# Performance work log

Hardware: AMD Instinct MI355X
Metric: run time of the kernel (lower is better)

The kernel has to match this reference:

```python
import jax, jax.numpy as jnp
import numpy as np

E = 8        # num_experts
TOP_K = 2
DIM = 1024
DFF = DIM // 4
T = 32768    # batch*seq tokens


def setup_inputs() -> dict:
    key = jax.random.key(0)
    ks = jax.random.split(key, 5)
    x = jax.random.normal(ks[0], (T, DIM), dtype=jnp.float32)
    router_w = jax.random.normal(ks[1], (E, DIM), dtype=jnp.float32) * 0.02
    w1 = jax.random.normal(ks[2], (E, DIM, DFF), dtype=jnp.float32) * 0.02
    w2 = jax.random.normal(ks[3], (E, DFF, DIM), dtype=jnp.float32) * 0.02
    w3 = jax.random.normal(ks[4], (E, DIM, DFF), dtype=jnp.float32) * 0.02
    return {"x": x, "router_w": router_w, "w1": w1, "w2": w2, "w3": w3}


def reference(x, router_w, w1, w2, w3):
    # ---- Router ----
    logits = x @ router_w.T                          # [T, E]
    scores = jax.nn.softmax(logits.astype(jnp.float32), axis=1)
    # expert_bias is zero at init and noise_scale=0 -> topk on raw scores
    _, sel = jax.lax.top_k(scores, TOP_K)            # [T, K] expert indices
    top_scores = jnp.take_along_axis(scores, sel, axis=-1)
    top_scores = top_scores / jnp.sum(top_scores, axis=-1, keepdims=True)

    flat_experts = sel.reshape(-1)                   # [T*K]
    sorted_idx = jnp.argsort(flat_experts)           # stable sort, expert-centric order
    scatter_idx = sorted_idx // TOP_K                # original token id per row
    num_tokens_per_expert = jnp.bincount(flat_experts, length=E).astype(jnp.int32)

    x_gathered = x[scatter_idx]                      # [T*K, DIM]
    scores_sorted = top_scores.reshape(-1)[sorted_idx]  # [T*K]

    # ---- GroupedExpert: grouped GEMM SwiGLU in bf16 ----
    xb = x_gathered.astype(jnp.bfloat16)
    x1 = jax.lax.ragged_dot(xb, w1.astype(jnp.bfloat16), num_tokens_per_expert)
    x3 = jax.lax.ragged_dot(xb, w3.astype(jnp.bfloat16), num_tokens_per_expert)
    h = jax.nn.silu(x1) * x3                         # [T*K, DFF] bf16
    expert_out = jax.lax.ragged_dot(h, w2.astype(jnp.bfloat16), num_tokens_per_expert)
    expert_out = expert_out.astype(x.dtype)          # [T*K, DIM]

    # ---- Combine: weighted scatter-add back to token positions ----
    out = jnp.zeros_like(x).at[scatter_idx].add(expert_out * scores_sorted[:, None])
    return out
```

## Files before the change

kernel.cpp:

```cpp
#include <hip/hip_runtime.h>
#include <cstdint>
#include <cstddef>
#include <math.h>

#define T_TOK 32768
#define DIM   1024
#define DFF   256
#define NE    8
#define NB    16
#define ROWS  (T_TOK * 2)
#define MAXROWS 66560
#define MAXTILES (MAXROWS / 64)

typedef unsigned short u16;
typedef __attribute__((ext_vector_type(8))) short v8s;
typedef __attribute__((ext_vector_type(4))) float v4f;

__device__ __forceinline__ u16 f2bf(float f) {
  union { float f; unsigned u; } v; v.f = f;
  return (u16)((v.u + 0x7FFFu + ((v.u >> 16) & 1u)) >> 16);
}
__device__ __forceinline__ float bf2f(u16 b) {
  union { unsigned u; float f; } v; v.u = ((unsigned)b) << 16; return v.f;
}

__device__ __forceinline__ void gload16(const u16* g, u16* l) {
  __builtin_amdgcn_global_load_lds(
      (const __attribute__((address_space(1))) void*)g,
      (__attribute__((address_space(3))) void*)l, 16, 0, 0);
}

#define WS_W13  ((size_t)0)
#define WS_W2T  ((size_t)8388608)
#define WS_H    ((size_t)12582912)
#define WS_Y    ((size_t)46661632)
#define WS_RTOK ((size_t)182976512)
#define WS_POS  ((size_t)183242752)
#define WS_CNT  ((size_t)183504896)
#define WS_CUR  ((size_t)183504960)
#define WS_OFF  ((size_t)183505024)
#define WS_SEL  ((size_t)183505152)
#define WS_WTS  ((size_t)183767296)
#define WS_XB   WS_Y

__global__ __launch_bounds__(256) void k_pack13(const float* __restrict__ w1,
                                                const float* __restrict__ w3,
                                                u16* __restrict__ W13p) {
  __shared__ float s1[32][33];
  __shared__ float s3[32][33];
  int e = blockIdx.z, k0 = blockIdx.x * 32, j0w = blockIdx.y;
  int tx = threadIdx.x, ty = threadIdx.y;
  size_t wbase = (size_t)e * DIM * DFF;
#pragma unroll
  for (int r = 0; r < 4; ++r) {
    int kl = ty + 8 * r;
    size_t src = wbase + (size_t)(k0 + kl) * DFF + j0w * 32 + tx;
    s1[kl][tx] = w1[src];
    s3[kl][tx] = w3[src];
  }
  __syncthreads();
  size_t obase = (size_t)e * 512 * 1024;
#pragma unroll
  for (int r = 0; r < 4; ++r) {
    int jl = ty + 8 * r;
    int n1 = 64 * j0w + jl;
    W13p[obase + (size_t)n1 * 1024 + k0 + tx]        = f2bf(s1[tx][jl]);
    W13p[obase + (size_t)(n1 + 32) * 1024 + k0 + tx] = f2bf(s3[tx][jl]);
  }
}

__global__ __launch_bounds__(256) void k_pack2(const float* __restrict__ w2,
                                               u16* __restrict__ W2t) {
  __shared__ float s[32][33];
  int e = blockIdx.z, k0 = blockIdx.x * 32, n0 = blockIdx.y * 32;
  int tx = threadIdx.x, ty = threadIdx.y;
#pragma unroll
  for (int r = 0; r < 4; ++r) {
    int kl = ty + 8 * r;
    s[kl][tx] = w2[(size_t)e * DFF * DIM + (size_t)(k0 + kl) * DIM + n0 + tx];
  }
  __syncthreads();
#pragma unroll
  for (int r = 0; r < 4; ++r) {
    int nl = ty + 8 * r;
    W2t[(size_t)e * DIM * DFF + (size_t)(n0 + nl) * DFF + k0 + tx] = f2bf(s[tx][nl]);
  }
}

__global__ __launch_bounds__(256) void k_router(const float* __restrict__ x,
                                                const float* __restrict__ rw,
                                                int* __restrict__ sel,
                                                float* __restrict__ wts,
                                                int* __restrict__ cnt,
                                                u16* __restrict__ xb) {
  __shared__ __align__(16) float s_rw[NE][1028];
  __shared__ __align__(16) float s_x[32][132];
  __shared__ float s_lg[256];
  __shared__ int s_cnt[NB];
  int tid = threadIdx.x;
  if (tid < NB) s_cnt[tid] = 0;
  {
    const float4* rw4 = (const float4*)rw;
#pragma unroll
    for (int r = 0; r < 8; ++r)
      *(float4*)(&s_rw[r][tid * 4]) = rw4[r * 256 + tid];
  }
  int tl = tid >> 3, e = tid & 7;
  float acc = 0.0f;
  const float4* x4 = (const float4*)x;
  for (int c = 0; c < 8; ++c) {
    __syncthreads();
#pragma unroll
    for (int j = 0; j < 4; ++j) {
      int slot = j * 256 + tid;
      int t = slot >> 5, kk = (slot & 31) * 4;
      *(float4*)(&s_x[t][kk]) = x4[((size_t)blockIdx.x * 32 + t) * 256 + c * 32 + (slot & 31)];
    }
    __syncthreads();
    const float* xp = &s_x[tl][0];
    const float* wp = &s_rw[e][c * 128];
#pragma unroll 16
    for (int k = 0; k < 128; ++k) acc = fmaf(xp[k], wp[k], acc);
    {
      int t2 = tid >> 3, k2 = (tid & 7) * 16;
      const float* sp = &s_x[t2][k2];
      u16 tb[16];
#pragma unroll
      for (int k = 0; k < 16; ++k) tb[k] = f2bf(sp[k]);
      u16* xo = xb + ((size_t)(blockIdx.x * 32 + t2)) * 1024 + c * 128 + k2;
      *(uint4*)(xo)     = *(const uint4*)(&tb[0]);
      *(uint4*)(xo + 8) = *(const uint4*)(&tb[8]);
    }
  }
  s_lg[tid] = acc;
  __syncthreads();
  if ((tid & 7) == 0) {
    int t = blockIdx.x * 32 + tl;
    const float* lg = s_lg + tid;
    int b0 = 0; float v0 = lg[0];
#pragma unroll
    for (int ee = 1; ee < NE; ++ee) if (lg[ee] > v0) { v0 = lg[ee]; b0 = ee; }
    int b1 = -1; float v1 = -1e30f;
#pragma unroll
    for (int ee = 0; ee < NE; ++ee) if (ee != b0 && lg[ee] > v1) { v1 = lg[ee]; b1 = ee; }
    float w0 = 1.0f / (1.0f + expf(v1 - v0));
    sel[2 * t] = b0; sel[2 * t + 1] = b1;
    wts[2 * t] = w0; wts[2 * t + 1] = 1.0f - w0;
    atomicAdd(&s_cnt[2 * b0], 1);
    atomicAdd(&s_cnt[2 * b1 + 1], 1);
  }
  __syncthreads();
  if (tid < NB && s_cnt[tid]) atomicAdd(&cnt[tid], s_cnt[tid]);
}

__global__ void k_scan(const int* __restrict__ cnt, int* __restrict__ offs) {
  if (threadIdx.x == 0 && blockIdx.x == 0) {
    int o = 0;
#pragma unroll
    for (int b = 0; b < NB; ++b) { offs[b] = o; o += (cnt[b] + 63) & ~63; }
    offs[NB] = o;
  }
}

__global__ __launch_bounds__(256) void k_scatter(const int* __restrict__ sel,
                                                 const int* __restrict__ offs,
                                                 int* __restrict__ cursor,
                                                 int* __restrict__ rtok,
                                                 int* __restrict__ pos) {
  __shared__ int s_cnt[NB], s_base[NB];
  int tid = threadIdx.x;
  if (tid < NB) s_cnt[tid] = 0;
  __syncthreads();
  int g = blockIdx.x * 256 + tid;
  int b = sel[g] * 2 + (g & 1);
  int lpos = atomicAdd(&s_cnt[b], 1);
  __syncthreads();
  if (tid < NB) s_base[tid] = s_cnt[tid] ? atomicAdd(&cursor[tid], s_cnt[tid]) : 0;
  __syncthreads();
  int row = offs[b] + s_base[b] + lpos;
  rtok[row] = g >> 1;
  pos[g] = row;
}

__global__ __launch_bounds__(512, 4) void k_gemm1(const u16* __restrict__ xb,
                                                  const u16* __restrict__ W13p,
                                                  const int* __restrict__ rtok,
                                                  const int* __restrict__ offs,
                                                  u16* __restrict__ h) {
  __shared__ __align__(16) u16 A_s[2][64][32];
  __shared__ __align__(16) u16 B_s[2][512][32];
  int bx = (int)((blockIdx.x & 7) * (MAXTILES / 8) + (blockIdx.x >> 3));
  int row0 = bx * 64;
  if (row0 >= offs[NB]) return;
  int b2 = 0;
  while (row0 >= offs[b2 + 1]) ++b2;
  int e = b2 >> 1;
  int tid = threadIdx.x;
  int wv = tid >> 6, lane = tid & 63;
  int lr = lane & 15, q = lane >> 4;
  int qa = q ^ ((lr >> 1) & 3);
  int srow = lane >> 2;
  int schk = (lane & 3) ^ ((lane >> 3) & 3);
  const u16* srcB = W13p + (size_t)e * 512 * 1024
                  + (size_t)(64 * wv + srow) * 1024 + schk * 8;
  int arow = (wv >= 4) ? (16 * (wv - 4) + srow) : srow;
  int tk = rtok[row0 + arow]; if (tk < 0) tk = 0;
  const u16* srcA = xb + (size_t)tk * 1024 + schk * 8;
  v4f acc[4][4] = {};

#define G1_STAGE(buf, k0) do {                                              \
    u16* ldsB_ = &B_s[buf][64 * wv][0];                                     \
    _Pragma("unroll")                                                       \
    for (int i_ = 0; i_ < 4; ++i_)                                          \
      gload16(srcB + (size_t)i_ * 16 * 1024 + (k0), ldsB_ + i_ * 512);      \
    if (wv >= 4) gload16(srcA + (k0), &A_s[buf][(wv & 3) * 16][0]);         \
  } while (0)

#define G1_COMP(buf) do {                                                   \
    v8s a_[4], b_[4];                                                       \
    _Pragma("unroll")                                                       \
    for (int mt_ = 0; mt_ < 4; ++mt_)                                       \
      a_[mt_] = *(const v8s*)(&A_s[buf][16 * mt_ + lr][qa * 8]);            \
    _Pragma("unroll")                                                       \
    for (int nt_ = 0; nt_ < 4; ++nt_)                                       \
      b_[nt_] = *(const v8s*)(&B_s[buf][64 * wv + 16 * nt_ + lr][qa * 8]);  \
    _Pragma("unroll")                                                       \
    for (int mt_ = 0; mt_ < 4; ++mt_)                                       \
      _Pragma("unroll")                                                     \
      for (int nt_ = 0; nt_ < 4; ++nt_)                                     \
        acc[mt_][nt_] = __builtin_amdgcn_mfma_f32_16x16x32_bf16(            \
            a_[mt_], b_[nt_], acc[mt_][nt_], 0, 0, 0);                      \
  } while (0)

  G1_STAGE(0, 0);
  asm volatile("s_waitcnt vmcnt(0)" ::: "memory");
  __builtin_amdgcn_s_barrier();
  __builtin_amdgcn_sched_barrier(0);
#pragma unroll 2
  for (int t = 0; t < 31; ++t) {
    int cur = t & 1;
    G1_STAGE(cur ^ 1, (t + 1) * 32);
    G1_COMP(cur);
    asm volatile("s_waitcnt vmcnt(0)" ::: "memory");
    __builtin_amdgcn_s_barrier();
    __builtin_amdgcn_sched_barrier(0);
  }
  G1_COMP(1);

#pragma unroll
  for (int mt = 0; mt < 4; ++mt)
#pragma unroll
    for (int nt = 0; nt < 2; ++nt)
#pragma unroll
      for (int r = 0; r < 4; ++r) {
        float x1 = bf2f(f2bf(acc[mt][nt][r]));
        float x3 = bf2f(f2bf(acc[mt][nt + 2][r]));
        float hv = x1 * x3 / (1.0f + __expf(-x1));
        int row = row0 + 16 * mt + q * 4 + r;
        int col = 32 * wv + 16 * nt + lr;
        h[(size_t)row * DFF + col] = f2bf(hv);
      }
#undef G1_STAGE
#undef G1_COMP
}

__global__ __launch_bounds__(512, 4) void k_gemm2(const u16* __restrict__ h,
                                                  const u16* __restrict__ W2t,
                                                  const int* __restrict__ offs,
                                                  u16* __restrict__ y) {
  __shared__ __align__(16) u16 A_s[2][64][32];
  __shared__ __align__(16) u16 B_s[2][512][32];
  int bx = (int)((blockIdx.x & 7) * (MAXTILES / 8) + (blockIdx.x >> 3));
  int row0 = bx * 64;
  if (row0 >= offs[NB]) return;
  int b2 = 0;
  while (row0 >= offs[b2 + 1]) ++b2;
  int e = b2 >> 1;
  int nb = blockIdx.y;
  int tid = threadIdx.x;
  int wv = tid >> 6, lane = tid & 63;
  int lr = lane & 15, q = lane >> 4;
  int qa = q ^ ((lr >> 1) & 3);
  int srow = lane >> 2;
  int schk = (lane & 3) ^ ((lane >> 3) & 3);
  const u16* srcB = W2t + (size_t)e * DIM * DFF + (size_t)nb * 512 * DFF
                  + (size_t)(64 * wv + srow) * DFF + schk * 8;
  int arow = (wv >= 4) ? (16 * (wv - 4) + srow) : srow;
  const u16* srcA = h + (size_t)(row0 + arow) * DFF + schk * 8;
  v4f acc[4][4] = {};

#define G2_STAGE(buf, k0) do {                                              \
    u16* ldsB_ = &B_s[buf][64 * wv][0];                                     \
    _Pragma("unroll")                                                       \
    for (int i_ = 0; i_ < 4; ++i_)                                          \
      gload16(srcB + (size_t)i_ * 16 * DFF + (k0), ldsB_ + i_ * 512);       \
    if (wv >= 4) gload16(srcA + (k0), &A_s[buf][(wv & 3) * 16][0]);         \
  } while (0)

#define G2_COMP(buf) do {                                                   \
    v8s a_[4], b_[4];                                                       \
    _Pragma("unroll")                                                       \
    for (int mt_ = 0; mt_ < 4; ++mt_)                                       \
      a_[mt_] = *(const v8s*)(&A_s[buf][16 * mt_ + lr][qa * 8]);            \
    _Pragma("unroll")                                                       \
    for (int nt_ = 0; nt_ < 4; ++nt_)                                       \
      b_[nt_] = *(const v8s*)(&B_s[buf][64 * wv + 16 * nt_ + lr][qa * 8]);  \
    _Pragma("unroll")                                                       \
    for (int mt_ = 0; mt_ < 4; ++mt_)                                       \
      _Pragma("unroll")                                                     \
      for (int nt_ = 0; nt_ < 4; ++nt_)                                     \
        acc[mt_][nt_] = __builtin_amdgcn_mfma_f32_16x16x32_bf16(            \
            a_[mt_], b_[nt_], acc[mt_][nt_], 0, 0, 0);                      \
  } while (0)

  G2_STAGE(0, 0);
  asm volatile("s_waitcnt vmcnt(0)" ::: "memory");
  __builtin_amdgcn_s_barrier();
  __builtin_amdgcn_sched_barrier(0);
#pragma unroll 2
  for (int t = 0; t < 7; ++t) {
    int cur = t & 1;
    G2_STAGE(cur ^ 1, (t + 1) * 32);
    G2_COMP(cur);
    asm volatile("s_waitcnt vmcnt(0)" ::: "memory");
    __builtin_amdgcn_s_barrier();
    __builtin_amdgcn_sched_barrier(0);
  }
  G2_COMP(1);
  __syncthreads();

  u16* Ts = &B_s[0][0][0];
#pragma unroll
  for (int mt = 0; mt < 4; ++mt) {
#pragma unroll
    for (int nt = 0; nt < 4; ++nt)
#pragma unroll
      for (int r = 0; r < 4; ++r)
        Ts[(q * 4 + r) * 520 + 64 * wv + 16 * nt + lr] = f2bf(acc[mt][nt][r]);
    __syncthreads();
#pragma unroll
    for (int i = 0; i < 2; ++i) {
      int j = tid + 512 * i;
      int rr = j >> 6, cc = j & 63;
      uint4 v = *(const uint4*)(Ts + rr * 520 + cc * 8);
      *(uint4*)(y + (size_t)(row0 + 16 * mt + rr) * 1024 + nb * 512 + cc * 8) = v;
    }
    __syncthreads();
  }
#undef G2_STAGE
#undef G2_COMP
}

__global__ __launch_bounds__(256) void k_combine(const u16* __restrict__ y,
                                                 const int* __restrict__ pos,
                                                 const float* __restrict__ wts,
                                                 float* __restrict__ out) {
  int tid = threadIdx.x, wv = tid >> 6, lane = tid & 63;
  int t = blockIdx.x * 4 + wv;
  int r0 = pos[2 * t], r1 = pos[2 * t + 1];
  float w0 = wts[2 * t], w1 = wts[2 * t + 1];
  const uint4* y0 = (const uint4*)(y + (size_t)r0 * 1024);
  const uint4* y1 = (const uint4*)(y + (size_t)r1 * 1024);
  float* o = out + (size_t)t * 1024;
#pragma unroll
  for (int i = 0; i < 2; ++i) {
    int j = lane + 64 * i;
    uint4 a = y0[j], b = y1[j];
    const u16* pa = (const u16*)&a;
    const u16* pb = (const u16*)&b;
    float f[8];
#pragma unroll
    for (int k = 0; k < 8; ++k) f[k] = bf2f(pa[k]) * w0 + bf2f(pb[k]) * w1;
    *(float4*)(o + j * 8)     = *(float4*)&f[0];
    *(float4*)(o + j * 8 + 4) = *(float4*)&f[4];
  }
}

extern "C" void kernel_launch(void* const* d_in, const int* in_sizes, int n_in,
                              void* d_out, int out_size, void* d_ws, size_t ws_size,
                              hipStream_t stream) {
  (void)in_sizes; (void)n_in; (void)ws_size; (void)out_size;
  const float* x  = (const float*)d_in[0];
  const float* rw = (const float*)d_in[1];
  const float* w1 = (const float*)d_in[2];
  const float* w2 = (const float*)d_in[3];
  const float* w3 = (const float*)d_in[4];
  float* out = (float*)d_out;
  char* ws = (char*)d_ws;
  u16*   W13p = (u16*)(ws + WS_W13);
  u16*   W2t  = (u16*)(ws + WS_W2T);
  u16*   hbuf = (u16*)(ws + WS_H);
  u16*   ybuf = (u16*)(ws + WS_Y);
  u16*   xbuf = (u16*)(ws + WS_XB);
  int*   rtok = (int*)(ws + WS_RTOK);
  int*   pos  = (int*)(ws + WS_POS);
  int*   cnt  = (int*)(ws + WS_CNT);
  int*   cur  = (int*)(ws + WS_CUR);
  int*   offs = (int*)(ws + WS_OFF);
  int*   sel  = (int*)(ws + WS_SEL);
  float* wts  = (float*)(ws + WS_WTS);

  hipMemsetAsync(ws + WS_RTOK, 0xFF, (size_t)MAXROWS * 4, stream);
  hipMemsetAsync(ws + WS_CNT, 0, 128, stream);

  k_pack13<<<dim3(32, 8, 8), dim3(32, 8), 0, stream>>>(w1, w3, W13p);
  k_pack2 <<<dim3(8, 32, 8), dim3(32, 8), 0, stream>>>(w2, W2t);
  k_router<<<dim3(T_TOK / 32), dim3(256), 0, stream>>>(x, rw, sel, wts, cnt, xbuf);
  k_scan  <<<dim3(1), dim3(64), 0, stream>>>(cnt, offs);
  k_scatter<<<dim3(ROWS / 256), dim3(256), 0, stream>>>(sel, offs, cur, rtok, pos);
  k_gemm1 <<<dim3(MAXTILES), dim3(512), 0, stream>>>(xbuf, W13p, rtok, offs, hbuf);
  k_gemm2 <<<dim3(MAXTILES, 2), dim3(512), 0, stream>>>(hbuf, W2t, offs, ybuf);
  k_combine<<<dim3(T_TOK / 4), dim3(256), 0, stream>>>(ybuf, pos, wts, out);
}
```

Measured before the change: 489.2 us.

## Retile grouped GEMMs to 128x128 blocks with paired 64-row tiles

Both expert GEMMs switch from 64-row x 512-col tiles on 512 threads to 128x128 tiles on 256 threads, with a 2x2 wave layout. Two adjacent 64-row tiles of the same expert bucket are merged into one block, and the odd partner exits early. The N dimension is split across more blocks (4 for gemm1, 8 for gemm2), which raises grid size and balances A/B reuse. The risk is that more blocks re-read the gathered activation rows, and that unpaired 64-row tails leave half the waves idle.

After: 578.9 us. +18.3%, slower.

```diff
diff --git a/kernel.cpp b/kernel.cpp
--- a/kernel.cpp
+++ b/kernel.cpp
@@ -182,48 +182,60 @@
   pos[g] = row;
 }
 
-__global__ __launch_bounds__(512, 4) void k_gemm1(const u16* __restrict__ xb,
+__global__ __launch_bounds__(256, 4) void k_gemm1(const u16* __restrict__ xb,
                                                   const u16* __restrict__ W13p,
                                                   const int* __restrict__ rtok,
                                                   const int* __restrict__ offs,
                                                   u16* __restrict__ h) {
-  __shared__ __align__(16) u16 A_s[2][64][32];
-  __shared__ __align__(16) u16 B_s[2][512][32];
+  __shared__ __align__(16) u16 A_s[2][128][32];
+  __shared__ __align__(16) u16 B_s[2][128][32];
   int bx = (int)((blockIdx.x & 7) * (MAXTILES / 8) + (blockIdx.x >> 3));
   int row0 = bx * 64;
-  if (row0 >= offs[NB]) return;
+  int totR = offs[NB];
+  if (row0 >= totR) return;
   int b2 = 0;
   while (row0 >= offs[b2 + 1]) ++b2;
   int e = b2 >> 1;
+  bool paired = (bx & 1) ? (row0 - 64 >= offs[b2]) : (row0 + 64 < offs[b2 + 1]);
+  if (paired && (bx & 1)) return;
+  int M = paired ? 128 : 64;
+  int nb = blockIdx.y;
   int tid = threadIdx.x;
   int wv = tid >> 6, lane = tid & 63;
+  int wr = wv >> 1, wc = wv & 1;
   int lr = lane & 15, q = lane >> 4;
   int qa = q ^ ((lr >> 1) & 3);
   int srow = lane >> 2;
   int schk = (lane & 3) ^ ((lane >> 3) & 3);
-  const u16* srcB = W13p + (size_t)e * 512 * 1024
-                  + (size_t)(64 * wv + srow) * 1024 + schk * 8;
-  int arow = (wv >= 4) ? (16 * (wv - 4) + srow) : srow;
-  int tk = rtok[row0 + arow]; if (tk < 0) tk = 0;
-  const u16* srcA = xb + (size_t)tk * 1024 + schk * 8;
+  const u16* srcA[2];
+  const u16* srcB[2];
+#pragma unroll
+  for (int i = 0; i < 2; ++i) {
+    int r = row0 + 32 * wv + 16 * i + srow;
+    if (r > MAXROWS - 1) r = MAXROWS - 1;
+    int tk = rtok[r];
+    if (tk < 0 || tk >= T_TOK) tk = 0;
+    srcA[i] = xb + (size_t)tk * 1024 + schk * 8;
+    int n = nb * 128 + 32 * wv + 16 * i + srow;
+    srcB[i] = W13p + (size_t)e * 512 * 1024 + (size_t)n * 1024 + schk * 8;
+  }
   v4f acc[4][4] = {};
 
 #define G1_STAGE(buf, k0) do {                                              \
-    u16* ldsB_ = &B_s[buf][64 * wv][0];                                     \
-    _Pragma("unroll")                                                       \
-    for (int i_ = 0; i_ < 4; ++i_)                                          \
-      gload16(srcB + (size_t)i_ * 16 * 1024 + (k0), ldsB_ + i_ * 512);      \
-    if (wv >= 4) gload16(srcA + (k0), &A_s[buf][(wv & 3) * 16][0]);         \
+    gload16(srcA[0] + (k0), &A_s[buf][32 * wv][0]);                         \
+    gload16(srcA[1] + (k0), &A_s[buf][32 * wv + 16][0]);                    \
+    gload16(srcB[0] + (k0), &B_s[buf][32 * wv][0]);                         \
+    gload16(srcB[1] + (k0), &B_s[buf][32 * wv + 16][0]);                    \
   } while (0)
 
 #define G1_COMP(buf) do {                                                   \
     v8s a_[4], b_[4];                                                       \
     _Pragma("unroll")                                                       \
     for (int mt_ = 0; mt_ < 4; ++mt_)                                       \
-      a_[mt_] = *(const v8s*)(&A_s[buf][16 * mt_ + lr][qa * 8]);            \
+      a_[mt_] = *(const v8s*)(&A_s[buf][64 * wr + 16 * mt_ + lr][qa * 8]);  \
     _Pragma("unroll")                                                       \
     for (int nt_ = 0; nt_ < 4; ++nt_)                                       \
-      b_[nt_] = *(const v8s*)(&B_s[buf][64 * wv + 16 * nt_ + lr][qa * 8]);  \
+      b_[nt_] = *(const v8s*)(&B_s[buf][64 * wc + 16 * nt_ + lr][qa * 8]);  \
     _Pragma("unroll")                                                       \
     for (int mt_ = 0; mt_ < 4; ++mt_)                                       \
       _Pragma("unroll")                                                     \
@@ -247,64 +259,75 @@
   }
   G1_COMP(1);
 
-#pragma unroll
-  for (int mt = 0; mt < 4; ++mt)
-#pragma unroll
-    for (int nt = 0; nt < 2; ++nt)
-#pragma unroll
-      for (int r = 0; r < 4; ++r) {
-        float x1 = bf2f(f2bf(acc[mt][nt][r]));
-        float x3 = bf2f(f2bf(acc[mt][nt + 2][r]));
-        float hv = x1 * x3 / (1.0f + __expf(-x1));
-        int row = row0 + 16 * mt + q * 4 + r;
-        int col = 32 * wv + 16 * nt + lr;
-        h[(size_t)row * DFF + col] = f2bf(hv);
-      }
+  if (M == 128 || wr == 0) {
+    int cb = 32 * (2 * nb + wc);
+#pragma unroll
+    for (int mt = 0; mt < 4; ++mt)
+#pragma unroll
+      for (int nt = 0; nt < 2; ++nt)
+#pragma unroll
+        for (int r = 0; r < 4; ++r) {
+          float x1 = bf2f(f2bf(acc[mt][nt][r]));
+          float x3 = bf2f(f2bf(acc[mt][nt + 2][r]));
+          float hv = x1 * x3 / (1.0f + __expf(-x1));
+          int row = row0 + 64 * wr + 16 * mt + q * 4 + r;
+          h[(size_t)row * DFF + cb + 16 * nt + lr] = f2bf(hv);
+        }
+  }
 #undef G1_STAGE
 #undef G1_COMP
 }
 
-__global__ __launch_bounds__(512, 4) void k_gemm2(const u16* __restrict__ h,
+__global__ __launch_bounds__(256, 4) void k_gemm2(const u16* __restrict__ h,
                                                   const u16* __restrict__ W2t,
                                                   const int* __restrict__ offs,
                                                   u16* __restrict__ y) {
-  __shared__ __align__(16) u16 A_s[2][64][32];
-  __shared__ __align__(16) u16 B_s[2][512][32];
+  __shared__ __align__(16) u16 A_s[2][128][32];
+  __shared__ __align__(16) u16 B_s[2][128][32];
   int bx = (int)((blockIdx.x & 7) * (MAXTILES / 8) + (blockIdx.x >> 3));
   int row0 = bx * 64;
-  if (row0 >= offs[NB]) return;
+  int totR = offs[NB];
+  if (row0 >= totR) return;
   int b2 = 0;
   while (row0 >= offs[b2 + 1]) ++b2;
   int e = b2 >> 1;
+  bool paired = (bx & 1) ? (row0 - 64 >= offs[b2]) : (row0 + 64 < offs[b2 + 1]);
+  if (paired && (bx & 1)) return;
+  int M = paired ? 128 : 64;
   int nb = blockIdx.y;
   int tid = threadIdx.x;
   int wv = tid >> 6, lane = tid & 63;
+  int wr = wv >> 1, wc = wv & 1;
   int lr = lane & 15, q = lane >> 4;
   int qa = q ^ ((lr >> 1) & 3);
   int srow = lane >> 2;
   int schk = (lane & 3) ^ ((lane >> 3) & 3);
-  const u16* srcB = W2t + (size_t)e * DIM * DFF + (size_t)nb * 512 * DFF
-                  + (size_t)(64 * wv + srow) * DFF + schk * 8;
-  int arow = (wv >= 4) ? (16 * (wv - 4) + srow) : srow;
-  const u16* srcA = h + (size_t)(row0 + arow) * DFF + schk * 8;
+  const u16* srcA[2];
+  const u16* srcB[2];
+#pragma unroll
+  for (int i = 0; i < 2; ++i) {
+    int r = row0 + 32 * wv + 16 * i + srow;
+    srcA[i] = h + (size_t)r * DFF + schk * 8;
+    int n = nb * 128 + 32 * wv + 16 * i + srow;
+    srcB[i] = W2t + (size_t)e * DIM * DFF + (size_t)n * DFF + schk * 8;
+  }
   v4f acc[4][4] = {};
 
 #define G2_STAGE(buf, k0) do {                                              \
-    u16* ldsB_ = &B_s[buf][64 * wv][0];                                     \
-    _Pragma("unroll")                                                       \
-    for (int i_ = 0; i_ < 4; ++i_)                                          \
-      gload16(srcB + (size_t)i_ * 16 * DFF + (k0), ldsB_ + i_ * 512);       \
-    if (wv >= 4) gload16(srcA + (k0), &A_s[buf][(wv & 3) * 16][0]);         \
+    gload16(srcA[0] + (k0), &A_s[buf][32 * wv][0]);                         \
+    gload16(srcA[1] + (k0), &A_s[buf][32 * wv + 16][0]);                    \
+    gload16(srcB[0] + (k0), &B_s[buf][32 * wv][0]);                         \
+    gload16(srcB[1] + (k0), &B_s[buf][32 * wv + 16][0]);                    \
   } while (0)
 
 #define G2_COMP(buf) do {                                                   \
     v8s a_[4], b_[4];                                                       \
     _Pragma("unroll")                                                       \
     for (int mt_ = 0; mt_ < 4; ++mt_)                                       \
-      a_[mt_] = *(const v8s*)(&A_s[buf][16 * mt_ + lr][qa * 8]);            \
+      a_[mt_] = *(const v8s*)(&A_s[buf][64 * wr + 16 * mt_ + lr][qa * 8]);  \
     _Pragma("unroll")                                                       \
     for (int nt_ = 0; nt_ < 4; ++nt_)                                       \
-      b_[nt_] = *(const v8s*)(&B_s[buf][64 * wv + 16 * nt_ + lr][qa * 8]);  \
+      b_[nt_] = *(const v8s*)(&B_s[buf][64 * wc + 16 * nt_ + lr][qa * 8]);  \
     _Pragma("unroll")                                                       \
     for (int mt_ = 0; mt_ < 4; ++mt_)                                       \
       _Pragma("unroll")                                                     \
@@ -329,21 +352,27 @@
   G2_COMP(1);
   __syncthreads();
 
-  u16* Ts = &B_s[0][0][0];
-#pragma unroll
-  for (int mt = 0; mt < 4; ++mt) {
-#pragma unroll
-    for (int nt = 0; nt < 4; ++nt)
-#pragma unroll
-      for (int r = 0; r < 4; ++r)
-        Ts[(q * 4 + r) * 520 + 64 * wv + 16 * nt + lr] = f2bf(acc[mt][nt][r]);
+  u16* Ts = &A_s[0][0][0];
+#pragma unroll
+  for (int j = 0; j < 4; ++j) {
+    if (M == 128 || wr == 0) {
+#pragma unroll
+      for (int nt = 0; nt < 4; ++nt)
+#pragma unroll
+        for (int r = 0; r < 4; ++r)
+          Ts[wr * 16 * 136 + (q * 4 + r) * 136 + 64 * wc + 16 * nt + lr] =
+              f2bf(acc[j][nt][r]);
+    }
     __syncthreads();
-#pragma unroll
-    for (int i = 0; i < 2; ++i) {
-      int j = tid + 512 * i;
-      int rr = j >> 6, cc = j & 63;
-      uint4 v = *(const uint4*)(Ts + rr * 520 + cc * 8);
-      *(uint4*)(y + (size_t)(row0 + 16 * mt + rr) * 1024 + nb * 512 + cc * 8) = v;
+    if (M == 128 || wr == 0) {
+#pragma unroll
+      for (int i = 0; i < 2; ++i) {
+        int u = wc * 64 + lane + 128 * i;
+        int rr = u >> 4, cc = u & 15;
+        uint4 v = *(const uint4*)(Ts + wr * 16 * 136 + rr * 136 + cc * 8);
+        int grow = row0 + 64 * wr + 16 * j + rr;
+        *(uint4*)(y + (size_t)grow * 1024 + nb * 128 + cc * 8) = v;
+      }
     }
     __syncthreads();
   }
@@ -408,7 +437,7 @@
   k_router<<<dim3(T_TOK / 32), dim3(256), 0, stream>>>(x, rw, sel, wts, cnt, xbuf);
   k_scan  <<<dim3(1), dim3(64), 0, stream>>>(cnt, offs);
   k_scatter<<<dim3(ROWS / 256), dim3(256), 0, stream>>>(sel, offs, cur, rtok, pos);
-  k_gemm1 <<<dim3(MAXTILES), dim3(512), 0, stream>>>(xbuf, W13p, rtok, offs, hbuf);
-  k_gemm2 <<<dim3(MAXTILES, 2), dim3(512), 0, stream>>>(hbuf, W2t, offs, ybuf);
+  k_gemm1 <<<dim3(MAXTILES, 4), dim3(256), 0, stream>>>(xbuf, W13p, rtok, offs, hbuf);
+  k_gemm2 <<<dim3(MAXTILES, 8), dim3(256), 0, stream>>>(hbuf, W2t, offs, ybuf);
   k_combine<<<dim3(T_TOK / 4), dim3(256), 0, stream>>>(ybuf, pos, wts, out);
 }
```

## Deepen GEMM pipelines to keep two loads in flight with split LDS reads

Applied to the files above, without the earlier changes.

Both grouped GEMM kernels now issue global-to-LDS loads two k-steps ahead. Each iteration first reads the current LDS buffer into registers, then synchronises, then reuses that same buffer for the prefetch. The waits drop from vmcnt(0) to vmcnt(5), so one stage of loads stays outstanding during the MFMA block, and s_setprio raises wave priority around the MFMAs. All eight waves now share the A-tile load, each issuing 5 loads per stage, which keeps the vmcnt counts uniform. The cost is an extra barrier per iteration and more live registers.

Result: no change. 487.8 us (-0.3%).

```diff
diff --git a/kernel.cpp b/kernel.cpp
--- a/kernel.cpp
+++ b/kernel.cpp
@@ -203,27 +203,30 @@
   int schk = (lane & 3) ^ ((lane >> 3) & 3);
   const u16* srcB = W13p + (size_t)e * 512 * 1024
                   + (size_t)(64 * wv + srow) * 1024 + schk * 8;
-  int arow = (wv >= 4) ? (16 * (wv - 4) + srow) : srow;
+  int arow = 16 * (wv & 3) + srow;
   int tk = rtok[row0 + arow]; if (tk < 0) tk = 0;
   const u16* srcA = xb + (size_t)tk * 1024 + schk * 8;
   v4f acc[4][4] = {};
+  v8s a_[4], b_[4];
 
 #define G1_STAGE(buf, k0) do {                                              \
     u16* ldsB_ = &B_s[buf][64 * wv][0];                                     \
     _Pragma("unroll")                                                       \
     for (int i_ = 0; i_ < 4; ++i_)                                          \
       gload16(srcB + (size_t)i_ * 16 * 1024 + (k0), ldsB_ + i_ * 512);      \
-    if (wv >= 4) gload16(srcA + (k0), &A_s[buf][(wv & 3) * 16][0]);         \
-  } while (0)
-
-#define G1_COMP(buf) do {                                                   \
-    v8s a_[4], b_[4];                                                       \
+    gload16(srcA + (k0), &A_s[buf][(wv & 3) * 16][0]);                      \
+  } while (0)
+
+#define G1_LOAD(buf) do {                                                   \
     _Pragma("unroll")                                                       \
     for (int mt_ = 0; mt_ < 4; ++mt_)                                       \
       a_[mt_] = *(const v8s*)(&A_s[buf][16 * mt_ + lr][qa * 8]);            \
     _Pragma("unroll")                                                       \
     for (int nt_ = 0; nt_ < 4; ++nt_)                                       \
       b_[nt_] = *(const v8s*)(&B_s[buf][64 * wv + 16 * nt_ + lr][qa * 8]);  \
+  } while (0)
+
+#define G1_MFMA() do {                                                      \
     _Pragma("unroll")                                                       \
     for (int mt_ = 0; mt_ < 4; ++mt_)                                       \
       _Pragma("unroll")                                                     \
@@ -233,19 +236,38 @@
   } while (0)
 
   G1_STAGE(0, 0);
+  G1_STAGE(1, 32);
+  asm volatile("s_waitcnt vmcnt(5)" ::: "memory");
+  __builtin_amdgcn_s_barrier();
+  __builtin_amdgcn_sched_barrier(0);
+#pragma unroll 2
+  for (int t = 0; t < 30; ++t) {
+    int cur = t & 1;
+    G1_LOAD(cur);
+    asm volatile("s_waitcnt lgkmcnt(0)" ::: "memory");
+    __builtin_amdgcn_sched_barrier(0);
+    __builtin_amdgcn_s_barrier();
+    __builtin_amdgcn_sched_barrier(0);
+    G1_STAGE(cur, (t + 2) * 32);
+    __builtin_amdgcn_sched_barrier(0);
+    __builtin_amdgcn_s_setprio(1);
+    G1_MFMA();
+    __builtin_amdgcn_s_setprio(0);
+    asm volatile("s_waitcnt vmcnt(5)" ::: "memory");
+    __builtin_amdgcn_s_barrier();
+    __builtin_amdgcn_sched_barrier(0);
+  }
+  G1_LOAD(0);
+  asm volatile("s_waitcnt lgkmcnt(0)" ::: "memory");
+  __builtin_amdgcn_sched_barrier(0);
+  G1_MFMA();
   asm volatile("s_waitcnt vmcnt(0)" ::: "memory");
   __builtin_amdgcn_s_barrier();
   __builtin_amdgcn_sched_barrier(0);
-#pragma unroll 2
-  for (int t = 0; t < 31; ++t) {
-    int cur = t & 1;
-    G1_STAGE(cur ^ 1, (t + 1) * 32);
-    G1_COMP(cur);
-    asm volatile("s_waitcnt vmcnt(0)" ::: "memory");
-    __builtin_amdgcn_s_barrier();
-    __builtin_amdgcn_sched_barrier(0);
-  }
-  G1_COMP(1);
+  G1_LOAD(1);
+  asm volatile("s_waitcnt lgkmcnt(0)" ::: "memory");
+  __builtin_amdgcn_sched_barrier(0);
+  G1_MFMA();
 
 #pragma unroll
   for (int mt = 0; mt < 4; ++mt)
@@ -261,7 +283,8 @@
         h[(size_t)row * DFF + col] = f2bf(hv);
       }
 #undef G1_STAGE
-#undef G1_COMP
+#undef G1_LOAD
+#undef G1_MFMA
 }
 
 __global__ __launch_bounds__(512, 4) void k_gemm2(const u16* __restrict__ h,
@@ -285,26 +308,29 @@
   int schk = (lane & 3) ^ ((lane >> 3) & 3);
   const u16* srcB = W2t + (size_t)e * DIM * DFF + (size_t)nb * 512 * DFF
                   + (size_t)(64 * wv + srow) * DFF + schk * 8;
-  int arow = (wv >= 4) ? (16 * (wv - 4) + srow) : srow;
+  int arow = 16 * (wv & 3) + srow;
   const u16* srcA = h + (size_t)(row0 + arow) * DFF + schk * 8;
   v4f acc[4][4] = {};
+  v8s a_[4], b_[4];
 
 #define G2_STAGE(buf, k0) do {                                              \
     u16* ldsB_ = &B_s[buf][64 * wv][0];                                     \
     _Pragma("unroll")                                                       \
     for (int i_ = 0; i_ < 4; ++i_)                                          \
       gload16(srcB + (size_t)i_ * 16 * DFF + (k0), ldsB_ + i_ * 512);       \
-    if (wv >= 4) gload16(srcA + (k0), &A_s[buf][(wv & 3) * 16][0]);         \
-  } while (0)
-
-#define G2_COMP(buf) do {                                                   \
-    v8s a_[4], b_[4];                                                       \
+    gload16(srcA + (k0), &A_s[buf][(wv & 3) * 16][0]);                      \
+  } while (0)
+
+#define G2_LOAD(buf) do {                                                   \
     _Pragma("unroll")                                                       \
     for (int mt_ = 0; mt_ < 4; ++mt_)                                       \
       a_[mt_] = *(const v8s*)(&A_s[buf][16 * mt_ + lr][qa * 8]);            \
     _Pragma("unroll")                                                       \
     for (int nt_ = 0; nt_ < 4; ++nt_)                                       \
       b_[nt_] = *(const v8s*)(&B_s[buf][64 * wv + 16 * nt_ + lr][qa * 8]);  \
+  } while (0)
+
+#define G2_MFMA() do {                                                      \
     _Pragma("unroll")                                                       \
     for (int mt_ = 0; mt_ < 4; ++mt_)                                       \
       _Pragma("unroll")                                                     \
@@ -314,19 +340,38 @@
   } while (0)
 
   G2_STAGE(0, 0);
+  G2_STAGE(1, 32);
+  asm volatile("s_waitcnt vmcnt(5)" ::: "memory");
+  __builtin_amdgcn_s_barrier();
+  __builtin_amdgcn_sched_barrier(0);
+#pragma unroll 2
+  for (int t = 0; t < 6; ++t) {
+    int cur = t & 1;
+    G2_LOAD(cur);
+    asm volatile("s_waitcnt lgkmcnt(0)" ::: "memory");
+    __builtin_amdgcn_sched_barrier(0);
+    __builtin_amdgcn_s_barrier();
+    __builtin_amdgcn_sched_barrier(0);
+    G2_STAGE(cur, (t + 2) * 32);
+    __builtin_amdgcn_sched_barrier(0);
+    __builtin_amdgcn_s_setprio(1);
+    G2_MFMA();
+    __builtin_amdgcn_s_setprio(0);
+    asm volatile("s_waitcnt vmcnt(5)" ::: "memory");
+    __builtin_amdgcn_s_barrier();
+    __builtin_amdgcn_sched_barrier(0);
+  }
+  G2_LOAD(0);
+  asm volatile("s_waitcnt lgkmcnt(0)" ::: "memory");
+  __builtin_amdgcn_sched_barrier(0);
+  G2_MFMA();
   asm volatile("s_waitcnt vmcnt(0)" ::: "memory");
   __builtin_amdgcn_s_barrier();
   __builtin_amdgcn_sched_barrier(0);
-#pragma unroll 2
-  for (int t = 0; t < 7; ++t) {
-    int cur = t & 1;
-    G2_STAGE(cur ^ 1, (t + 1) * 32);
-    G2_COMP(cur);
-    asm volatile("s_waitcnt vmcnt(0)" ::: "memory");
-    __builtin_amdgcn_s_barrier();
-    __builtin_amdgcn_sched_barrier(0);
-  }
-  G2_COMP(1);
+  G2_LOAD(1);
+  asm volatile("s_waitcnt lgkmcnt(0)" ::: "memory");
+  __builtin_amdgcn_sched_barrier(0);
+  G2_MFMA();
   __syncthreads();
 
   u16* Ts = &B_s[0][0][0];
@@ -348,7 +393,8 @@
     __syncthreads();
   }
 #undef G2_STAGE
-#undef G2_COMP
+#undef G2_LOAD
+#undef G2_MFMA
 }
 
 __global__ __launch_bounds__(256) void k_combine(const u16* __restrict__ y,
```

## Restructure grouped GEMMs: A operand in registers, per-wave private LDS, no block barriers

Applied to the files above, without the earlier changes.

Both grouped GEMM kernels now use 256-thread blocks with twice as many column blocks. Each wave loads its A fragments straight from global memory into registers and keeps a private double-buffered LDS slice for its B tile. Because no LDS is shared between waves, the per-iteration block barriers become per-wave waitcnts, and the gemm2 epilogue transposes through per-wave LDS without __syncthreads. The aim is to drop barrier stalls and shared A staging, at the cost of redundant A loads across waves and more register pressure.

After: 581.5 us. +18.9%, slower.

```diff
diff --git a/kernel.cpp b/kernel.cpp
--- a/kernel.cpp
+++ b/kernel.cpp
@@ -182,19 +182,21 @@
   pos[g] = row;
 }
 
-__global__ __launch_bounds__(512, 4) void k_gemm1(const u16* __restrict__ xb,
+__global__ __launch_bounds__(256, 3) void k_gemm1(const u16* __restrict__ xb,
                                                   const u16* __restrict__ W13p,
                                                   const int* __restrict__ rtok,
                                                   const int* __restrict__ offs,
                                                   u16* __restrict__ h) {
-  __shared__ __align__(16) u16 A_s[2][64][32];
-  __shared__ __align__(16) u16 B_s[2][512][32];
+  __shared__ __align__(16) u16 Bs[4][2][64][32];
   int bx = (int)((blockIdx.x & 7) * (MAXTILES / 8) + (blockIdx.x >> 3));
   int row0 = bx * 64;
   if (row0 >= offs[NB]) return;
   int b2 = 0;
-  while (row0 >= offs[b2 + 1]) ++b2;
+#pragma unroll
+  for (int bb = 0; bb < NB - 1; ++bb)
+    if (row0 >= offs[bb + 1]) b2 = bb + 1;
   int e = b2 >> 1;
+  int by = blockIdx.y;
   int tid = threadIdx.x;
   int wv = tid >> 6, lane = tid & 63;
   int lr = lane & 15, q = lane >> 4;
@@ -202,153 +204,212 @@
   int srow = lane >> 2;
   int schk = (lane & 3) ^ ((lane >> 3) & 3);
   const u16* srcB = W13p + (size_t)e * 512 * 1024
-                  + (size_t)(64 * wv + srow) * 1024 + schk * 8;
-  int arow = (wv >= 4) ? (16 * (wv - 4) + srow) : srow;
-  int tk = rtok[row0 + arow]; if (tk < 0) tk = 0;
-  const u16* srcA = xb + (size_t)tk * 1024 + schk * 8;
+                  + (size_t)(by * 256 + 64 * wv + srow) * 1024 + schk * 8;
+  u16* buf0 = &Bs[wv][0][0][0];
+  u16* buf1 = &Bs[wv][1][0][0];
+  const u16* srcA[4];
+#pragma unroll
+  for (int mt = 0; mt < 4; ++mt) {
+    int tk = rtok[row0 + 16 * mt + lr];
+    if (tk < 0) tk = 0;
+    srcA[mt] = xb + (size_t)tk * 1024 + q * 8;
+  }
+  uint4 areg[2][4];
+  v8s b_[4];
   v4f acc[4][4] = {};
 
-#define G1_STAGE(buf, k0) do {                                              \
-    u16* ldsB_ = &B_s[buf][64 * wv][0];                                     \
+#define G1_ALOAD(P, k0) do {                                                \
+    _Pragma("unroll")                                                       \
+    for (int mt_ = 0; mt_ < 4; ++mt_)                                       \
+      areg[P][mt_] = *(const uint4*)(srcA[mt_] + (k0));                     \
+  } while (0)
+#define G1_STAGE(dst, k0) do {                                              \
     _Pragma("unroll")                                                       \
     for (int i_ = 0; i_ < 4; ++i_)                                          \
-      gload16(srcB + (size_t)i_ * 16 * 1024 + (k0), ldsB_ + i_ * 512);      \
-    if (wv >= 4) gload16(srcA + (k0), &A_s[buf][(wv & 3) * 16][0]);         \
-  } while (0)
-
-#define G1_COMP(buf) do {                                                   \
-    v8s a_[4], b_[4];                                                       \
-    _Pragma("unroll")                                                       \
-    for (int mt_ = 0; mt_ < 4; ++mt_)                                       \
-      a_[mt_] = *(const v8s*)(&A_s[buf][16 * mt_ + lr][qa * 8]);            \
+      gload16(srcB + (size_t)i_ * 16 * 1024 + (k0), (dst) + i_ * 512);      \
+  } while (0)
+#define G1_BREAD(src) do {                                                  \
     _Pragma("unroll")                                                       \
     for (int nt_ = 0; nt_ < 4; ++nt_)                                       \
-      b_[nt_] = *(const v8s*)(&B_s[buf][64 * wv + 16 * nt_ + lr][qa * 8]);  \
-    _Pragma("unroll")                                                       \
-    for (int mt_ = 0; mt_ < 4; ++mt_)                                       \
+      b_[nt_] = *(const v8s*)((src) + (16 * nt_ + lr) * 32 + qa * 8);       \
+    asm volatile("s_waitcnt lgkmcnt(0)" ::: "memory");                      \
+    __builtin_amdgcn_sched_barrier(0);                                      \
+  } while (0)
+#define G1_MFMA(P) do {                                                     \
+    _Pragma("unroll")                                                       \
+    for (int mt_ = 0; mt_ < 4; ++mt_) {                                     \
+      v8s a_ = *(const v8s*)(&areg[P][mt_]);                                \
       _Pragma("unroll")                                                     \
       for (int nt_ = 0; nt_ < 4; ++nt_)                                     \
         acc[mt_][nt_] = __builtin_amdgcn_mfma_f32_16x16x32_bf16(            \
-            a_[mt_], b_[nt_], acc[mt_][nt_], 0, 0, 0);                      \
-  } while (0)
-
-  G1_STAGE(0, 0);
+            a_, b_[nt_], acc[mt_][nt_], 0, 0, 0);                           \
+    }                                                                       \
+  } while (0)
+#define G1_ITER(P, sb, rb, tt) do {                                         \
+    G1_MFMA(P);                                                             \
+    G1_ALOAD(P, (tt + 2) * 32);                                             \
+    G1_STAGE(sb, (tt + 2) * 32);                                            \
+    asm volatile("s_waitcnt vmcnt(8)" ::: "memory");                        \
+    __builtin_amdgcn_sched_barrier(0);                                      \
+    G1_BREAD(rb);                                                           \
+  } while (0)
+
+  G1_ALOAD(0, 0);
+  G1_STAGE(buf0, 0);
+  __builtin_amdgcn_sched_barrier(0);
+  G1_ALOAD(1, 32);
+  G1_STAGE(buf1, 32);
+  asm volatile("s_waitcnt vmcnt(8)" ::: "memory");
+  __builtin_amdgcn_sched_barrier(0);
+  G1_BREAD(buf0);
+
+  for (int t = 0; t < 30; t += 2) {
+    G1_ITER(0, buf0, buf1, t);
+    G1_ITER(1, buf1, buf0, t + 1);
+  }
+  G1_MFMA(0);
   asm volatile("s_waitcnt vmcnt(0)" ::: "memory");
-  __builtin_amdgcn_s_barrier();
-  __builtin_amdgcn_sched_barrier(0);
-#pragma unroll 2
-  for (int t = 0; t < 31; ++t) {
-    int cur = t & 1;
-    G1_STAGE(cur ^ 1, (t + 1) * 32);
-    G1_COMP(cur);
-    asm volatile("s_waitcnt vmcnt(0)" ::: "memory");
-    __builtin_amdgcn_s_barrier();
-    __builtin_amdgcn_sched_barrier(0);
-  }
-  G1_COMP(1);
-
-#pragma unroll
-  for (int mt = 0; mt < 4; ++mt)
-#pragma unroll
-    for (int nt = 0; nt < 2; ++nt)
-#pragma unroll
-      for (int r = 0; r < 4; ++r) {
-        float x1 = bf2f(f2bf(acc[mt][nt][r]));
-        float x3 = bf2f(f2bf(acc[mt][nt + 2][r]));
-        float hv = x1 * x3 / (1.0f + __expf(-x1));
-        int row = row0 + 16 * mt + q * 4 + r;
-        int col = 32 * wv + 16 * nt + lr;
-        h[(size_t)row * DFF + col] = f2bf(hv);
-      }
+  __builtin_amdgcn_sched_barrier(0);
+  G1_BREAD(buf1);
+  G1_MFMA(1);
+
+  {
+    int cb = 128 * by + 32 * wv;
+#pragma unroll
+    for (int mt = 0; mt < 4; ++mt)
+#pragma unroll
+      for (int nt = 0; nt < 2; ++nt)
+#pragma unroll
+        for (int r = 0; r < 4; ++r) {
+          float x1 = bf2f(f2bf(acc[mt][nt][r]));
+          float x3 = bf2f(f2bf(acc[mt][nt + 2][r]));
+          float hv = x1 * x3 / (1.0f + __expf(-x1));
+          int row = row0 + 16 * mt + q * 4 + r;
+          h[(size_t)row * DFF + cb + 16 * nt + lr] = f2bf(hv);
+        }
+  }
+#undef G1_ALOAD
 #undef G1_STAGE
-#undef G1_COMP
-}
-
-__global__ __launch_bounds__(512, 4) void k_gemm2(const u16* __restrict__ h,
+#undef G1_BREAD
+#undef G1_MFMA
+#undef G1_ITER
+}
+
+__global__ __launch_bounds__(256, 3) void k_gemm2(const u16* __restrict__ h,
                                                   const u16* __restrict__ W2t,
                                                   const int* __restrict__ offs,
                                                   u16* __restrict__ y) {
-  __shared__ __align__(16) u16 A_s[2][64][32];
-  __shared__ __align__(16) u16 B_s[2][512][32];
+  __shared__ __align__(16) u16 Bs[4][2][64][32];
   int bx = (int)((blockIdx.x & 7) * (MAXTILES / 8) + (blockIdx.x >> 3));
   int row0 = bx * 64;
   if (row0 >= offs[NB]) return;
   int b2 = 0;
-  while (row0 >= offs[b2 + 1]) ++b2;
+#pragma unroll
+  for (int bb = 0; bb < NB - 1; ++bb)
+    if (row0 >= offs[bb + 1]) b2 = bb + 1;
   int e = b2 >> 1;
-  int nb = blockIdx.y;
+  int by = blockIdx.y;
   int tid = threadIdx.x;
   int wv = tid >> 6, lane = tid & 63;
   int lr = lane & 15, q = lane >> 4;
   int qa = q ^ ((lr >> 1) & 3);
   int srow = lane >> 2;
   int schk = (lane & 3) ^ ((lane >> 3) & 3);
-  const u16* srcB = W2t + (size_t)e * DIM * DFF + (size_t)nb * 512 * DFF
-                  + (size_t)(64 * wv + srow) * DFF + schk * 8;
-  int arow = (wv >= 4) ? (16 * (wv - 4) + srow) : srow;
-  const u16* srcA = h + (size_t)(row0 + arow) * DFF + schk * 8;
+  const u16* srcB = W2t + (size_t)e * DIM * DFF
+                  + (size_t)(by * 256 + 64 * wv + srow) * DFF + schk * 8;
+  u16* buf0 = &Bs[wv][0][0][0];
+  u16* buf1 = &Bs[wv][1][0][0];
+  const u16* srcA[4];
+#pragma unroll
+  for (int mt = 0; mt < 4; ++mt)
+    srcA[mt] = h + (size_t)(row0 + 16 * mt + lr) * DFF + q * 8;
+  uint4 areg[2][4];
+  v8s b_[4];
   v4f acc[4][4] = {};
 
-#define G2_STAGE(buf, k0) do {                                              \
-    u16* ldsB_ = &B_s[buf][64 * wv][0];                                     \
+#define G2_ALOAD(P, k0) do {                                                \
+    _Pragma("unroll")                                                       \
+    for (int mt_ = 0; mt_ < 4; ++mt_)                                       \
+      areg[P][mt_] = *(const uint4*)(srcA[mt_] + (k0));                     \
+  } while (0)
+#define G2_STAGE(dst, k0) do {                                              \
     _Pragma("unroll")                                                       \
     for (int i_ = 0; i_ < 4; ++i_)                                          \
-      gload16(srcB + (size_t)i_ * 16 * DFF + (k0), ldsB_ + i_ * 512);       \
-    if (wv >= 4) gload16(srcA + (k0), &A_s[buf][(wv & 3) * 16][0]);         \
-  } while (0)
-
-#define G2_COMP(buf) do {                                                   \
-    v8s a_[4], b_[4];                                                       \
-    _Pragma("unroll")                                                       \
-    for (int mt_ = 0; mt_ < 4; ++mt_)                                       \
-      a_[mt_] = *(const v8s*)(&A_s[buf][16 * mt_ + lr][qa * 8]);            \
+      gload16(srcB + (size_t)i_ * 16 * DFF + (k0), (dst) + i_ * 512);       \
+  } while (0)
+#define G2_BREAD(src) do {                                                  \
     _Pragma("unroll")                                                       \
     for (int nt_ = 0; nt_ < 4; ++nt_)                                       \
-      b_[nt_] = *(const v8s*)(&B_s[buf][64 * wv + 16 * nt_ + lr][qa * 8]);  \
-    _Pragma("unroll")                                                       \
-    for (int mt_ = 0; mt_ < 4; ++mt_)                                       \
+      b_[nt_] = *(const v8s*)((src) + (16 * nt_ + lr) * 32 + qa * 8);       \
+    asm volatile("s_waitcnt lgkmcnt(0)" ::: "memory");                      \
+    __builtin_amdgcn_sched_barrier(0);                                      \
+  } while (0)
+#define G2_MFMA(P) do {                                                     \
+    _Pragma("unroll")                                                       \
+    for (int mt_ = 0; mt_ < 4; ++mt_) {                                     \
+      v8s a_ = *(const v8s*)(&areg[P][mt_]);                                \
       _Pragma("unroll")                                                     \
       for (int nt_ = 0; nt_ < 4; ++nt_)                                     \
         acc[mt_][nt_] = __builtin_amdgcn_mfma_f32_16x16x32_bf16(            \
-            a_[mt_], b_[nt_], acc[mt_][nt_], 0, 0, 0);                      \
-  } while (0)
-
-  G2_STAGE(0, 0);
+            a_, b_[nt_], acc[mt_][nt_], 0, 0, 0);                           \
+    }                                                                       \
+  } while (0)
+#define G2_ITER(P, sb, rb, tt) do {                                         \
+    G2_MFMA(P);                                                             \
+    G2_ALOAD(P, (tt + 2) * 32);                                             \
+    G2_STAGE(sb, (tt + 2) * 32);                                            \
+    asm volatile("s_waitcnt vmcnt(8)" ::: "memory");                        \
+    __builtin_amdgcn_sched_barrier(0);                                      \
+    G2_BREAD(rb);                                                           \
+  } while (0)
+
+  G2_ALOAD(0, 0);
+  G2_STAGE(buf0, 0);
+  __builtin_amdgcn_sched_barrier(0);
+  G2_ALOAD(1, 32);
+  G2_STAGE(buf1, 32);
+  asm volatile("s_waitcnt vmcnt(8)" ::: "memory");
+  __builtin_amdgcn_sched_barrier(0);
+  G2_BREAD(buf0);
+
+  for (int t = 0; t < 6; t += 2) {
+    G2_ITER(0, buf0, buf1, t);
+    G2_ITER(1, buf1, buf0, t + 1);
+  }
+  G2_MFMA(0);
   asm volatile("s_waitcnt vmcnt(0)" ::: "memory");
-  __builtin_amdgcn_s_barrier();
-  __builtin_amdgcn_sched_barrier(0);
-#pragma unroll 2
-  for (int t = 0; t < 7; ++t) {
-    int cur = t & 1;
-    G2_STAGE(cur ^ 1, (t + 1) * 32);
-    G2_COMP(cur);
-    asm volatile("s_waitcnt vmcnt(0)" ::: "memory");
-    __builtin_amdgcn_s_barrier();
-    __builtin_amdgcn_sched_barrier(0);
-  }
-  G2_COMP(1);
-  __syncthreads();
-
-  u16* Ts = &B_s[0][0][0];
-#pragma unroll
-  for (int mt = 0; mt < 4; ++mt) {
-#pragma unroll
-    for (int nt = 0; nt < 4; ++nt)
-#pragma unroll
-      for (int r = 0; r < 4; ++r)
-        Ts[(q * 4 + r) * 520 + 64 * wv + 16 * nt + lr] = f2bf(acc[mt][nt][r]);
-    __syncthreads();
-#pragma unroll
-    for (int i = 0; i < 2; ++i) {
-      int j = tid + 512 * i;
-      int rr = j >> 6, cc = j & 63;
-      uint4 v = *(const uint4*)(Ts + rr * 520 + cc * 8);
-      *(uint4*)(y + (size_t)(row0 + 16 * mt + rr) * 1024 + nb * 512 + cc * 8) = v;
+  __builtin_amdgcn_sched_barrier(0);
+  G2_BREAD(buf1);
+  G2_MFMA(1);
+
+  {
+    u16* Ts = buf0;
+    int cb = by * 256 + 64 * wv;
+#pragma unroll
+    for (int mt = 0; mt < 4; ++mt) {
+#pragma unroll
+      for (int nt = 0; nt < 4; ++nt)
+#pragma unroll
+        for (int r = 0; r < 4; ++r)
+          Ts[(q * 4 + r) * 72 + 16 * nt + lr] = f2bf(acc[mt][nt][r]);
+      asm volatile("s_waitcnt lgkmcnt(0)" ::: "memory");
+      __builtin_amdgcn_sched_barrier(0);
+#pragma unroll
+      for (int i = 0; i < 2; ++i) {
+        int u = lane + 64 * i;
+        int rr = u >> 3, cc = u & 7;
+        uint4 v = *(const uint4*)(Ts + rr * 72 + cc * 8);
+        *(uint4*)(y + (size_t)(row0 + 16 * mt + rr) * 1024 + cb + cc * 8) = v;
+      }
+      asm volatile("s_waitcnt lgkmcnt(0)" ::: "memory");
+      __builtin_amdgcn_sched_barrier(0);
     }
-    __syncthreads();
-  }
+  }
+#undef G2_ALOAD
 #undef G2_STAGE
-#undef G2_COMP
+#undef G2_BREAD
+#undef G2_MFMA
+#undef G2_ITER
 }
 
 __global__ __launch_bounds__(256) void k_combine(const u16* __restrict__ y,
@@ -408,7 +469,7 @@
   k_router<<<dim3(T_TOK / 32), dim3(256), 0, stream>>>(x, rw, sel, wts, cnt, xbuf);
   k_scan  <<<dim3(1), dim3(64), 0, stream>>>(cnt, offs);
   k_scatter<<<dim3(ROWS / 256), dim3(256), 0, stream>>>(sel, offs, cur, rtok, pos);
-  k_gemm1 <<<dim3(MAXTILES), dim3(512), 0, stream>>>(xbuf, W13p, rtok, offs, hbuf);
-  k_gemm2 <<<dim3(MAXTILES, 2), dim3(512), 0, stream>>>(hbuf, W2t, offs, ybuf);
+  k_gemm1 <<<dim3(MAXTILES, 2), dim3(256), 0, stream>>>(xbuf, W13p, rtok, offs, hbuf);
+  k_gemm2 <<<dim3(MAXTILES, 4), dim3(256), 0, stream>>>(hbuf, W2t, offs, ybuf);
   k_combine<<<dim3(T_TOK / 4), dim3(256), 0, stream>>>(ybuf, pos, wts, out);
 }
```
